# Performance work log

Hardware: AMD Instinct MI355X
Metric: run time of the kernel (lower is better)

The kernel has to match this reference:

```python
import jax, jax.numpy as jnp
import numpy as np

NF = 64        # feature channels (nf == inter_channels == in_channels)
BURST = 14     # burst_size from Args
H = 128
W = 128
SCALE = 0.02   # weight init scale keeps softmax logits in a sane range


def conv1x1(x, w, b):
    # x: [B,C,H,W], w: [O,C], b: [O]
    return jnp.einsum('bchw,oc->bohw', x, w) + b[None, :, None, None]


def setup_inputs() -> dict:
    key = jax.random.key(0)
    ks = jax.random.split(key, 32)
    inp = {'aligned_fea': jax.random.normal(ks[0], (BURST, NF, H, W), dtype=jnp.float32)}
    names = ['gc', 'thc', 'phc', 'Wc', 'gh', 'thh', 'phh', 'Wh', 'gw', 'thw', 'phw', 'Ww']
    for i, n in enumerate(names):
        inp[n + '_w'] = SCALE * jax.random.normal(ks[1 + 2 * i], (NF, NF), dtype=jnp.float32)
        inp[n + '_b'] = SCALE * jax.random.normal(ks[2 + 2 * i], (NF,), dtype=jnp.float32)
    inp['fus_w'] = SCALE * jax.random.normal(ks[26], (NF, BURST * NF * 3), dtype=jnp.float32)
    inp['fus_b'] = SCALE * jax.random.normal(ks[27], (NF,), dtype=jnp.float32)
    return inp


def _forward(aligned_fea,
             gc_w, gc_b, thc_w, thc_b, phc_w, phc_b, Wc_w, Wc_b,
             gh_w, gh_b, thh_w, thh_b, phh_w, phh_b, Wh_w, Wh_b,
             gw_w, gw_b, thw_w, thw_b, phw_w, phw_b, Ww_w, Ww_b,
             fus_w, fus_b):
    B, C, h, w = aligned_fea.shape  # [14, 64, 128, 128]
    x = aligned_fea
    ref = aligned_fea[0:1]  # [1,C,H,W]

    # ---- channel non-local (self) ----
    g = conv1x1(x, gc_w, gc_b).reshape(B, C, h * w)
    th = conv1x1(x, thc_w, thc_b).reshape(B, C, h * w)
    ph = conv1x1(x, phc_w, phc_b).reshape(B, C, h * w)
    f = jnp.einsum('bcn,bdn->bcd', th, ph)            # [B,C,C]
    f = jax.nn.softmax(f, axis=1)                     # softmax over dim=1 as in torch
    y = jnp.einsum('bcd,bdn->bcn', f, g)              # [B,C,HW]
    y = jnp.transpose(y, (0, 2, 1)).reshape(B, C, h, w)  # permute+view as in torch
    zc = conv1x1(y, Wc_w, Wc_b) + x

    # ---- height non-local (cross with ref) ----
    g = conv1x1(x, gh_w, gh_b).reshape(B, h, C * w)
    th = conv1x1(ref, thh_w, thh_b).reshape(1, h, C * w)
    ph = conv1x1(x, phh_w, phh_b).reshape(B, h, C * w)
    f = jnp.einsum('bik,bjk->bij', jnp.broadcast_to(th, (B, h, C * w)), ph)  # [B,H,H]
    f = jax.nn.softmax(f, axis=1)
    y = jnp.einsum('bij,bjk->bik', f, g)              # [B,H,C*W]
    y = jnp.transpose(y, (0, 2, 1)).reshape(B, C, h, w)  # requires H == W
    zh = conv1x1(y, Wh_w, Wh_b) + x

    # ---- width non-local (cross with ref) ----
    g = conv1x1(x, gw_w, gw_b).reshape(B, w, C * h)
    th = conv1x1(ref, thw_w, thw_b).reshape(1, w, C * h)
    ph = conv1x1(x, phw_w, phw_b).reshape(B, w, C * h)
    f = jnp.einsum('bik,bjk->bij', jnp.broadcast_to(th, (B, w, C * h)), ph)  # [B,W,W]
    f = jax.nn.softmax(f, axis=1)
    y = jnp.einsum('bij,bjk->bik', f, g)              # [B,W,C*H]
    y = jnp.transpose(y, (0, 2, 1)).reshape(B, C, h, w)
    zw = conv1x1(y, Ww_w, Ww_b) + x

    # ---- fusion: cat frames along channel in order [c, h, w] ----
    feat = jnp.concatenate([zc.reshape(1, B * C, h, w),
                            zh.reshape(1, B * C, h, w),
                            zw.reshape(1, B * C, h, w)], axis=1)  # [1, 3*B*C, H, W]
    out = conv1x1(feat, fus_w, fus_b)
    return jnp.where(out >= 0, out, 0.2 * out)  # LeakyReLU(0.2)


def reference(aligned_fea,
              gc_w, gc_b, thc_w, thc_b, phc_w, phc_b, Wc_w, Wc_b,
              gh_w, gh_b, thh_w, thh_b, phh_w, phh_b, Wh_w, Wh_b,
              gw_w, gw_b, thw_w, thw_b, phw_w, phw_b, Ww_w, Ww_b,
              fus_w, fus_b):
    return _forward(aligned_fea,
                    gc_w, gc_b, thc_w, thc_b, phc_w, phc_b, Wc_w, Wc_b,
                    gh_w, gh_b, thh_w, thh_b, phh_w, phh_b, Wh_w, Wh_b,
                    gw_w, gw_b, thw_w, thw_b, phw_w, phw_b, Ww_w, Ww_b,
                    fus_w, fus_b)
```

## Files before the change

kernel.cpp:

```cpp
#include <hip/hip_runtime.h>

#define NF 64
#define BURST 14
#define NPIX 16384
#define CN (NF * NPIX)
#define LP 72

typedef short bf16x8 __attribute__((ext_vector_type(8)));
typedef float f32x4 __attribute__((ext_vector_type(4)));
typedef unsigned short us4 __attribute__((ext_vector_type(4)));

__device__ inline unsigned short f2bf(float f) {
    unsigned int u = __float_as_uint(f);
    return (unsigned short)((u + 0x7fffu + ((u >> 16) & 1u)) >> 16);
}
__device__ inline float bf2f(unsigned short u) {
    return __uint_as_float(((unsigned int)u) << 16);
}

__global__ __launch_bounds__(256) void cast_x(const float* __restrict__ X,
                                              unsigned short* __restrict__ XB,
                                              unsigned short* __restrict__ XT,
                                              float* __restrict__ S)
{
    __shared__ unsigned short Xs[128][LP];
    const int tid = threadIdx.x;
    const int p0 = blockIdx.x * 128;
    const int b = blockIdx.y;
    const size_t boff = (size_t)b * CN;
#pragma unroll
    for (int i = 0; i < 8; ++i) {
        const int id = tid + 256 * i;
        const int c = id >> 5, p4 = (id & 31) * 4;
        float4 v = *(const float4*)&X[boff + (size_t)c * NPIX + p0 + p4];
        us4 r;
        r.x = f2bf(v.x); r.y = f2bf(v.y); r.z = f2bf(v.z); r.w = f2bf(v.w);
        *(us4*)&XB[boff + (size_t)c * NPIX + p0 + p4] = r;
        Xs[p4 + 0][c] = r.x; Xs[p4 + 1][c] = r.y;
        Xs[p4 + 2][c] = r.z; Xs[p4 + 3][c] = r.w;
    }
    __syncthreads();
#pragma unroll
    for (int i = 0; i < 4; ++i) {
        const int id = tid + 256 * i;
        const int row = id >> 3, c8 = (id & 7) * 8;
        *(bf16x8*)&XT[boff + (size_t)(p0 + row) * 64 + c8] = *(const bf16x8*)&Xs[row][c8];
    }
    if (tid < 64) {
        float sv = 0.f;
        for (int pp = 0; pp < 128; ++pp) sv += bf2f(Xs[pp][tid]);
        atomicAdd(&S[(b * 2 + (p0 >= 8192 ? 1 : 0)) * 64 + tid], sv);
    }
}

__global__ __launch_bounds__(256) void precompute(
    const float* __restrict__ fus_w, const float* __restrict__ fus_b,
    const float* __restrict__ Wc, const float* __restrict__ bWc,
    const float* __restrict__ Wh, const float* __restrict__ bWh,
    const float* __restrict__ Ww, const float* __restrict__ bWw,
    const float* __restrict__ gcw, const float* __restrict__ ghw,
    const float* __restrict__ gww,
    unsigned short* __restrict__ M16, unsigned short* __restrict__ Wc16,
    float* __restrict__ cb, unsigned short* __restrict__ gT16)
{
    const int blk = blockIdx.x, tid = threadIdx.x;
    if (blk < 42) {
        __shared__ float Fl[64][65];
        __shared__ float Wl[64][65];
        const int g = blk / 14, b = blk % 14;
        const float* Wg = (g == 0) ? Wc : (g == 1) ? Wh : Ww;
#pragma unroll
        for (int i = 0; i < 4; ++i) {
            const int id = tid + 256 * i;
            const int r = id >> 4, c4 = (id & 15) * 4;
            float4 v = *(const float4*)&fus_w[r * 2688 + g * 896 + b * 64 + c4];
            Fl[r][c4] = v.x; Fl[r][c4 + 1] = v.y; Fl[r][c4 + 2] = v.z; Fl[r][c4 + 3] = v.w;
            float4 u = *(const float4*)&Wg[r * 64 + c4];
            Wl[r][c4] = u.x; Wl[r][c4 + 1] = u.y; Wl[r][c4 + 2] = u.z; Wl[r][c4 + 3] = u.w;
        }
        __syncthreads();
        const int o = tid & 63, qq = tid >> 6;
        float s[16];
#pragma unroll
        for (int i = 0; i < 16; ++i) s[i] = 0.f;
        for (int c2 = 0; c2 < 64; ++c2) {
            const float fv = Fl[o][c2];
#pragma unroll
            for (int i = 0; i < 16; ++i) s[i] += fv * Wl[c2][qq * 16 + i];
        }
        unsigned short* Mout = M16 + (size_t)blk * 4096;
#pragma unroll
        for (int i = 0; i < 16; i += 4) {
            us4 r4; r4.x = f2bf(s[i]); r4.y = f2bf(s[i + 1]); r4.z = f2bf(s[i + 2]); r4.w = f2bf(s[i + 3]);
            *(us4*)&Mout[o * 64 + qq * 16 + i] = r4;
        }
    } else if (blk < 98) {
        const int e0 = (blk - 42) * 1024 + tid * 4;
        const int o = e0 / 896, bc = e0 - o * 896;
        float4 a = *(const float4*)&fus_w[o * 2688 + bc];
        float4 b2 = *(const float4*)&fus_w[o * 2688 + 896 + bc];
        float4 c3 = *(const float4*)&fus_w[o * 2688 + 1792 + bc];
        us4 r;
        r.x = f2bf(a.x + b2.x + c3.x); r.y = f2bf(a.y + b2.y + c3.y);
        r.z = f2bf(a.z + b2.z + c3.z); r.w = f2bf(a.w + b2.w + c3.w);
        *(us4*)&Wc16[e0] = r;
    } else if (blk < 106) {
        __shared__ float red[256];
        const int o = (blk - 98) * 8 + (tid >> 5);
        const int lane = tid & 31;
        float s = 0.f;
        for (int t = 0; t < 84; ++t) {
            const int ch = lane + 32 * t;
            const int g = ch / 896, c2 = ch & 63;
            const float bg = (g == 0) ? bWc[c2] : (g == 1) ? bWh[c2] : bWw[c2];
            s += fus_w[o * 2688 + ch] * bg;
        }
        red[tid] = s;
        __syncthreads();
        if (tid < 8) {
            const int oo = (blk - 98) * 8 + tid;
            float t = fus_b[oo];
            for (int i = 0; i < 32; ++i) t += red[tid * 32 + i];
            cb[oo] = t;
        }
    } else {
        const int g = blk - 106;
        const float* wg = (g == 0) ? gcw : (g == 1) ? ghw : gww;
        unsigned short* dst = gT16 + (size_t)g * 4096;
        for (int e = tid; e < 4096; e += 256) {
            const int cp = e >> 6, d = e & 63;
            dst[e] = f2bf(wg[d * 64 + cp]);
        }
    }
}

__global__ __launch_bounds__(256) void gram(
    const unsigned short* __restrict__ XB, float* __restrict__ G)
{
    const int tid = threadIdx.x;
    const int w = tid >> 6, l = tid & 63, lm = l & 15, q = l >> 4;
    const int b = blockIdx.y, z = blockIdx.z;
    const unsigned short* A;
    const unsigned short* B;
    int k0, ksteps;
    if (z == 0) {
        A = XB + (size_t)b * CN; B = A;
        k0 = blockIdx.x * 2048; ksteps = 64;
    } else {
        const int dl = (z - 1) >> 1, dp = (z - 1) & 1;
        A = XB + (size_t)dl * 8192;
        B = XB + (size_t)b * CN + (size_t)dp * 8192;
        k0 = blockIdx.x * 1024; ksteps = 32;
    }
    const int mo = (w & 1) * 32, no = (w >> 1) * 32;
    f32x4 acc[2][2] = {};
    for (int ks = 0; ks < ksteps; ++ks) {
        const int k = k0 + ks * 32 + q * 8;
        bf16x8 a[2], bb[2];
#pragma unroll
        for (int mi = 0; mi < 2; ++mi) a[mi] = *(const bf16x8*)&A[(size_t)(mo + mi * 16 + lm) * NPIX + k];
#pragma unroll
        for (int ni = 0; ni < 2; ++ni) bb[ni] = *(const bf16x8*)&B[(size_t)(no + ni * 16 + lm) * NPIX + k];
#pragma unroll
        for (int mi = 0; mi < 2; ++mi)
#pragma unroll
            for (int ni = 0; ni < 2; ++ni)
                acc[mi][ni] = __builtin_amdgcn_mfma_f32_16x16x32_bf16(a[mi], bb[ni], acc[mi][ni], 0, 0, 0);
    }
    float* Gp = G + (size_t)(b * 5 + z) * 4096;
#pragma unroll
    for (int mi = 0; mi < 2; ++mi)
#pragma unroll
        for (int r = 0; r < 4; ++r)
#pragma unroll
            for (int ni = 0; ni < 2; ++ni)
                atomicAdd(&Gp[(mo + mi * 16 + q * 4 + r) * 64 + no + ni * 16 + lm], acc[mi][ni][r]);
}

__global__ __launch_bounds__(256) void sandwich(
    const float* __restrict__ thc_w, const float* __restrict__ phc_w,
    const float* __restrict__ thc_b, const float* __restrict__ phc_b,
    const float* __restrict__ thh_w, const float* __restrict__ phh_w,
    const float* __restrict__ thh_b, const float* __restrict__ phh_b,
    const float* __restrict__ thw_w, const float* __restrict__ phw_w,
    const float* __restrict__ thw_b, const float* __restrict__ phw_b,
    const float* __restrict__ G, const float* __restrict__ S,
    float* __restrict__ f1, float* __restrict__ f2)
{
    __shared__ float Wt[64][65], Wp[64][65], Gl[64][65], Tl[64][65];
    __shared__ float sth[64], sph[64], uu[64], vv[64], btl[64], bpl[64];
    const int b = blockIdx.x, y = blockIdx.y, tid = threadIdx.x;
    const float *Wth_g, *Wph_g, *bth_g, *bph_g, *Gp;
    float* outp; int dl = 0, dp = 0; float Kn;
    if (y == 0) {
        Wth_g = thc_w; Wph_g = phc_w; bth_g = thc_b; bph_g = phc_b;
        Gp = G + (size_t)(b * 5) * 4096; Kn = 16384.f;
        outp = f1 + (size_t)b * 4096;
    } else {
        const int part = (y - 1) / 4, e = (y - 1) & 3;
        dl = e >> 1; dp = e & 1;
        if (part == 0) { Wth_g = thh_w; Wph_g = phh_w; bth_g = thh_b; bph_g = phh_b; }
        else           { Wth_g = thw_w; Wph_g = phw_w; bth_g = thw_b; bph_g = phw_b; }
        Gp = G + (size_t)(b * 5 + 1 + e) * 4096; Kn = 8192.f;
        outp = f2 + (size_t)(part * 14 + b) * 16384;
    }
#pragma unroll
    for (int i = 0; i < 4; ++i) {
        const int id = tid + 256 * i;
        const int r = id >> 4, c4 = (id & 15) * 4;
        float4 v = *(const float4*)&Wth_g[r * 64 + c4];
        Wt[r][c4] = v.x; Wt[r][c4 + 1] = v.y; Wt[r][c4 + 2] = v.z; Wt[r][c4 + 3] = v.w;
        float4 u = *(const float4*)&Wph_g[r * 64 + c4];
        Wp[r][c4] = u.x; Wp[r][c4 + 1] = u.y; Wp[r][c4 + 2] = u.z; Wp[r][c4 + 3] = u.w;
        float4 g = *(const float4*)&Gp[r * 64 + c4];
        Gl[r][c4] = g.x; Gl[r][c4 + 1] = g.y; Gl[r][c4 + 2] = g.z; Gl[r][c4 + 3] = g.w;
    }
    if (tid < 64) {
        if (y == 0) { const float sf = S[b * 128 + tid] + S[b * 128 + 64 + tid]; sth[tid] = sf; sph[tid] = sf; }
        else { sth[tid] = S[dl * 64 + tid]; sph[tid] = S[b * 128 + dp * 64 + tid]; }
        btl[tid] = bth_g[tid]; bpl[tid] = bph_g[tid];
    }
    __syncthreads();
    if (tid < 64) {
        float su = 0.f, sv = 0.f;
        for (int c = 0; c < 64; ++c) { su += Wt[tid][c] * sth[c]; sv += Wp[tid][c] * sph[c]; }
        uu[tid] = su; vv[tid] = sv;
    }
    const int t = tid & 63, qq = tid >> 6;
    float r16[16];
#pragma unroll
    for (int i = 0; i < 16; ++i) r16[i] = 0.f;
    for (int c = 0; c < 64; ++c) {
        const float fv = Wt[t][c];
#pragma unroll
        for (int i = 0; i < 16; ++i) r16[i] += fv * Gl[c][qq * 16 + i];
    }
#pragma unroll
    for (int i = 0; i < 16; ++i) Tl[t][qq * 16 + i] = r16[i];
    __syncthreads();
#pragma unroll
    for (int i = 0; i < 16; ++i) r16[i] = 0.f;
    for (int c = 0; c < 64; ++c) {
        const float tv = Tl[t][c];
#pragma unroll
        for (int i = 0; i < 16; ++i) r16[i] += tv * Wp[qq * 16 + i][c];
    }
    if (y == 0) {
#pragma unroll
        for (int i = 0; i < 16; ++i) {
            const int d = qq * 16 + i;
            outp[t * 64 + d] = r16[i] + uu[t] * bpl[d] + btl[t] * vv[d] + Kn * btl[t] * bpl[d];
        }
    } else {
#pragma unroll
        for (int i = 0; i < 16; ++i) {
            const int tp = qq * 16 + i;
            outp[(2 * t + dl) * 128 + 2 * tp + dp] =
                r16[i] + uu[t] * bpl[tp] + btl[t] * vv[tp] + Kn * btl[t] * bpl[tp];
        }
    }
}

__global__ __launch_bounds__(256) void softmax_all(
    const float* __restrict__ f1, const float* __restrict__ f2,
    const float* __restrict__ gcb, const float* __restrict__ ghb,
    const float* __restrict__ gwb,
    unsigned short* __restrict__ o1, unsigned short* __restrict__ o2d,
    float* __restrict__ B1, float* __restrict__ B2)
{
    __shared__ float red[256];
    __shared__ float mxA[128], invA[128];
    __shared__ float bgl[64];
    const int bx = blockIdx.x, tid = threadIdx.x;
    if (bx < 14) {
        const float* Fb = f1 + (size_t)bx * 4096;
        unsigned short* Ob = o1 + (size_t)bx * 4096;
        if (tid < 64) bgl[tid] = gcb[tid];
        const int d = tid & 63, qq = tid >> 6;
        float mx = -1e30f;
        for (int c = qq * 16; c < qq * 16 + 16; ++c) mx = fmaxf(mx, Fb[c * 64 + d]);
        red[tid] = mx;
        __syncthreads();
        if (tid < 64) mxA[tid] = fmaxf(fmaxf(red[tid], red[64 + tid]), fmaxf(red[128 + tid], red[192 + tid]));
        __syncthreads();
        const float m = mxA[d];
        float s = 0.f;
        for (int c = qq * 16; c < qq * 16 + 16; ++c) s += __expf(Fb[c * 64 + d] - m);
        red[tid] = s;
        __syncthreads();
        if (tid < 64) invA[tid] = 1.f / (red[tid] + red[64 + tid] + red[128 + tid] + red[192 + tid]);
        __syncthreads();
        const int e0 = tid * 16;
        const int d0 = e0 & 63;
        float bp = 0.f;
#pragma unroll
        for (int i = 0; i < 16; i += 4) {
            us4 r4;
            float v0 = __expf(Fb[e0 + i] - mxA[d0 + i]) * invA[d0 + i];
            float v1 = __expf(Fb[e0 + i + 1] - mxA[d0 + i + 1]) * invA[d0 + i + 1];
            float v2 = __expf(Fb[e0 + i + 2] - mxA[d0 + i + 2]) * invA[d0 + i + 2];
            float v3 = __expf(Fb[e0 + i + 3] - mxA[d0 + i + 3]) * invA[d0 + i + 3];
            bp += v0 * bgl[d0 + i] + v1 * bgl[d0 + i + 1] + v2 * bgl[d0 + i + 2] + v3 * bgl[d0 + i + 3];
            r4.x = f2bf(v0); r4.y = f2bf(v1); r4.z = f2bf(v2); r4.w = f2bf(v3);
            *(us4*)&Ob[e0 + i] = r4;
        }
        red[tid] = bp;
        __syncthreads();
        if (tid < 64)
            B1[bx * 64 + tid] = red[tid * 4] + red[tid * 4 + 1] + red[tid * 4 + 2] + red[tid * 4 + 3];
    } else {
        const int idx = bx - 14;
        const float* Fb = f2 + (size_t)idx * 16384;
        if (tid < 64) bgl[tid] = (idx < 14) ? ghb[tid] : gwb[tid];
        const int j = tid & 127, ih = tid >> 7;
        float mx = -1e30f;
        for (int i = ih * 64; i < ih * 64 + 64; ++i) mx = fmaxf(mx, Fb[i * 128 + j]);
        red[tid] = mx;
        __syncthreads();
        if (tid < 128) mxA[tid] = fmaxf(red[tid], red[128 + tid]);
        __syncthreads();
        const float m = mxA[j];
        float s = 0.f;
        for (int i = ih * 64; i < ih * 64 + 64; ++i) s += __expf(Fb[i * 128 + j] - m);
        red[tid] = s;
        __syncthreads();
        if (tid < 128) invA[tid] = 1.f / (red[tid] + red[128 + tid]);
        __syncthreads();
        const int e0 = tid * 64;
        const int irow = tid >> 1;
        const int j0 = e0 & 127;
        unsigned short vt[2][32];
        float bp = 0.f;
        for (int ii = 0; ii < 64; ++ii) {
            const int jj = j0 + ii;
            const float v = __expf(Fb[e0 + ii] - mxA[jj]) * invA[jj];
            bp += v * bgl[jj >> 1];
            vt[jj & 1][ii >> 1] = f2bf(v);
        }
        unsigned short* Od = o2d + (size_t)idx * 16384 + irow * 64 + (j0 >> 1);
#pragma unroll
        for (int dlt = 0; dlt < 2; ++dlt)
#pragma unroll
            for (int ss = 0; ss < 32; ss += 4)
                *(us4*)&Od[dlt * 8192 + ss] = *(us4*)&vt[dlt][ss];
        red[tid] = bp;
        __syncthreads();
        if (tid < 128) B2[idx * 128 + tid] = red[2 * tid] + red[2 * tid + 1];
    }
}

__global__ __launch_bounds__(256) void kmat(
    const unsigned short* __restrict__ f16_1, const unsigned short* __restrict__ f2d,
    const unsigned short* __restrict__ gT16,
    unsigned short* __restrict__ K1, unsigned short* __restrict__ K2)
{
    const int b = blockIdx.x, y = blockIdx.y, tid = threadIdx.x;
    const int w = tid >> 6, l = tid & 63, lm = l & 15, q = l >> 4;
    if (y == 0) {
        const unsigned short* A = f16_1 + (size_t)b * 4096;
        const unsigned short* Bm = gT16;
        const int mo = (w & 1) * 32, no = (w >> 1) * 32;
        f32x4 acc[2][2] = {};
#pragma unroll
        for (int ks = 0; ks < 2; ++ks) {
            const int k = ks * 32 + q * 8;
            bf16x8 a[2], bb[2];
#pragma unroll
            for (int mi = 0; mi < 2; ++mi) a[mi] = *(const bf16x8*)&A[(mo + mi * 16 + lm) * 64 + k];
#pragma unroll
            for (int ni = 0; ni < 2; ++ni) bb[ni] = *(const bf16x8*)&Bm[(no + ni * 16 + lm) * 64 + k];
#pragma unroll
            for (int mi = 0; mi < 2; ++mi)
#pragma unroll
                for (int ni = 0; ni < 2; ++ni)
                    acc[mi][ni] = __builtin_amdgcn_mfma_f32_16x16x32_bf16(a[mi], bb[ni], acc[mi][ni], 0, 0, 0);
        }
        unsigned short* Kp = K1 + (size_t)b * 4096;
#pragma unroll
        for (int mi = 0; mi < 2; ++mi)
#pragma unroll
            for (int r = 0; r < 4; ++r)
#pragma unroll
                for (int ni = 0; ni < 2; ++ni)
                    Kp[(mo + mi * 16 + q * 4 + r) * 64 + no + ni * 16 + lm] = f2bf(acc[mi][ni][r]);
    } else {
        const int part = y - 1;
        const unsigned short* Bm = gT16 + (size_t)(1 + part) * 4096;
        unsigned short* Kp = K2 + (size_t)(part * 14 + b) * 16384;
        for (int dlt = 0; dlt < 2; ++dlt) {
            const unsigned short* A = f2d + (size_t)(part * 14 + b) * 16384 + dlt * 8192;
            const int mo = (w & 1) * 64, no = (w >> 1) * 32;
            f32x4 acc[4][2] = {};
#pragma unroll
            for (int ks = 0; ks < 2; ++ks) {
                const int k = ks * 32 + q * 8;
                bf16x8 a[4], bb[2];
#pragma unroll
                for (int mi = 0; mi < 4; ++mi) a[mi] = *(const bf16x8*)&A[(mo + mi * 16 + lm) * 64 + k];
#pragma unroll
                for (int ni = 0; ni < 2; ++ni) bb[ni] = *(const bf16x8*)&Bm[(no + ni * 16 + lm) * 64 + k];
#pragma unroll
                for (int mi = 0; mi < 4; ++mi)
#pragma unroll
                    for (int ni = 0; ni < 2; ++ni)
                        acc[mi][ni] = __builtin_amdgcn_mfma_f32_16x16x32_bf16(a[mi], bb[ni], acc[mi][ni], 0, 0, 0);
            }
#pragma unroll
            for (int mi = 0; mi < 4; ++mi)
#pragma unroll
                for (int r = 0; r < 4; ++r)
#pragma unroll
                    for (int ni = 0; ni < 2; ++ni)
                        Kp[dlt * 8192 + (mo + mi * 16 + q * 4 + r) * 64 + no + ni * 16 + lm] = f2bf(acc[mi][ni][r]);
        }
    }
}

__global__ __launch_bounds__(256) void fold_res(
    const unsigned short* __restrict__ Wcomb, const unsigned short* __restrict__ XT,
    float* __restrict__ Out)
{
    const int tid = threadIdx.x;
    const int w = tid >> 6, l = tid & 63, lm = l & 15, q = l >> 4;
    const int p0 = blockIdx.x * 64 + (w >> 1) * 32;
    const int oh = (w & 1) * 32;
    f32x4 acc[2][2] = {};
    for (int b = 0; b < 14; ++b) {
#pragma unroll
        for (int ks = 0; ks < 2; ++ks) {
            const int c0 = ks * 32 + q * 8;
            bf16x8 a[2], bb[2];
#pragma unroll
            for (int mi = 0; mi < 2; ++mi)
                a[mi] = *(const bf16x8*)&Wcomb[(oh + mi * 16 + lm) * 896 + b * 64 + c0];
#pragma unroll
            for (int ni = 0; ni < 2; ++ni)
                bb[ni] = *(const bf16x8*)&XT[(size_t)b * CN + (size_t)(p0 + ni * 16 + lm) * 64 + c0];
#pragma unroll
            for (int mi = 0; mi < 2; ++mi)
#pragma unroll
                for (int ni = 0; ni < 2; ++ni)
                    acc[mi][ni] = __builtin_amdgcn_mfma_f32_16x16x32_bf16(a[mi], bb[ni], acc[mi][ni], 0, 0, 0);
        }
    }
#pragma unroll
    for (int mi = 0; mi < 2; ++mi)
#pragma unroll
        for (int r = 0; r < 4; ++r) {
            const int o = oh + mi * 16 + q * 4 + r;
#pragma unroll
            for (int ni = 0; ni < 2; ++ni)
                Out[(size_t)o * NPIX + p0 + ni * 16 + lm] = acc[mi][ni][r];
        }
}

__global__ __launch_bounds__(256) void pv1k(
    const unsigned short* __restrict__ XT, const unsigned short* __restrict__ K1,
    const float* __restrict__ B1, unsigned short* __restrict__ Y)
{
    const int tid = threadIdx.x;
    const int w = tid >> 6, l = tid & 63, lm = l & 15, q = l >> 4;
    const int b = blockIdx.z;
    const int p0 = blockIdx.x * 256 + w * 64;
    const unsigned short* Xb = XT + (size_t)b * CN;
    const unsigned short* Kb = K1 + (size_t)b * 4096;
    f32x4 acc[4][4] = {};
#pragma unroll
    for (int ks = 0; ks < 2; ++ks) {
        const int c0 = ks * 32 + q * 8;
        bf16x8 a[4], bb[4];
#pragma unroll
        for (int mi = 0; mi < 4; ++mi) a[mi] = *(const bf16x8*)&Xb[(size_t)(p0 + mi * 16 + lm) * 64 + c0];
#pragma unroll
        for (int ni = 0; ni < 4; ++ni) bb[ni] = *(const bf16x8*)&Kb[(ni * 16 + lm) * 64 + c0];
#pragma unroll
        for (int mi = 0; mi < 4; ++mi)
#pragma unroll
            for (int ni = 0; ni < 4; ++ni)
                acc[mi][ni] = __builtin_amdgcn_mfma_f32_16x16x32_bf16(a[mi], bb[ni], acc[mi][ni], 0, 0, 0);
    }
    unsigned short* Yb = Y + (size_t)b * CN;
#pragma unroll
    for (int mi = 0; mi < 4; ++mi)
#pragma unroll
        for (int r = 0; r < 4; ++r) {
            const int p = p0 + mi * 16 + q * 4 + r;
#pragma unroll
            for (int ni = 0; ni < 4; ++ni) {
                const int c = ni * 16 + lm;
                Yb[(size_t)p * 64 + c] = f2bf(acc[mi][ni][r] + B1[b * 64 + c]);
            }
        }
}

__global__ __launch_bounds__(256) void pv23k(
    const unsigned short* __restrict__ XT, const unsigned short* __restrict__ K2,
    const float* __restrict__ B2, unsigned short* __restrict__ Y2,
    unsigned short* __restrict__ Y3)
{
    const int tid = threadIdx.x;
    const int w = tid >> 6, l = tid & 63, lm = l & 15, q = l >> 4;
    const int part = blockIdx.z / 14, b = blockIdx.z % 14;
    const int k00 = blockIdx.x * 256 + w * 64;
    const int i0 = blockIdx.y * 64;
    const unsigned short* Xb = XT + (size_t)b * CN;
    const unsigned short* Kb = K2 + (size_t)(part * 14 + b) * 16384;
    const float* Bb = B2 + (part * 14 + b) * 128;
    f32x4 acc[4][4] = {};
#pragma unroll
    for (int dlt = 0; dlt < 2; ++dlt) {
#pragma unroll
        for (int ks = 0; ks < 2; ++ks) {
            const int c0 = ks * 32 + q * 8;
            bf16x8 a[4], bb[4];
#pragma unroll
            for (int mi = 0; mi < 4; ++mi)
                a[mi] = *(const bf16x8*)&Xb[(size_t)(dlt * 8192 + k00 + mi * 16 + lm) * 64 + c0];
#pragma unroll
            for (int ni = 0; ni < 4; ++ni)
                bb[ni] = *(const bf16x8*)&Kb[dlt * 8192 + (i0 + ni * 16 + lm) * 64 + c0];
#pragma unroll
            for (int mi = 0; mi < 4; ++mi)
#pragma unroll
                for (int ni = 0; ni < 4; ++ni)
                    acc[mi][ni] = __builtin_amdgcn_mfma_f32_16x16x32_bf16(a[mi], bb[ni], acc[mi][ni], 0, 0, 0);
        }
    }
    unsigned short* Yb = (part ? Y3 : Y2) + (size_t)b * CN;
#pragma unroll
    for (int mi = 0; mi < 4; ++mi)
#pragma unroll
        for (int r = 0; r < 4; ++r) {
            const int k = k00 + mi * 16 + q * 4 + r;
#pragma unroll
            for (int ni = 0; ni < 4; ++ni) {
                const int ii = i0 + ni * 16 + lm;
                Yb[(size_t)k * 128 + ii] = f2bf(acc[mi][ni][r] + Bb[ii]);
            }
        }
}

__global__ __launch_bounds__(256) void yfold(
    const unsigned short* __restrict__ M16,
    const unsigned short* __restrict__ Y1, const unsigned short* __restrict__ Y2,
    const unsigned short* __restrict__ Y3, float* __restrict__ Out)
{
    __shared__ unsigned short As[64][LP];
    __shared__ unsigned short Ss[128][LP];
    const int tid = threadIdx.x;
    const int z = blockIdx.z;
    const unsigned short* Ap = M16 + (size_t)z * 14 * 4096;
    const unsigned short* S = (z == 0) ? Y1 : (z == 1) ? Y2 : Y3;
    const int p0 = blockIdx.x * 128;
    const int t0 = blockIdx.y * 7;
    const int w = tid >> 6, l = tid & 63, lm = l & 15, q = l >> 4;
    const int mo = (w & 1) * 32;
    const int no = (w >> 1) * 64;
    f32x4 acc[2][4] = {};

    for (int t = t0; t < t0 + 7; ++t) {
        __syncthreads();
#pragma unroll
        for (int i = 0; i < 2; ++i) {
            const int ch = tid + 256 * i;
            const int row = ch >> 3, c8 = (ch & 7) * 8;
            *(bf16x8*)&As[row][c8] = *(const bf16x8*)&Ap[(size_t)t * 4096 + (size_t)row * 64 + c8];
        }
#pragma unroll
        for (int i = 0; i < 4; ++i) {
            const int id = tid + 256 * i;
            const int c = id & 63, p8 = (id >> 6) * 8;
            bf16x8 v = *(const bf16x8*)&S[(size_t)t * CN + (size_t)c * NPIX + p0 + p8];
#pragma unroll
            for (int j = 0; j < 8; ++j) Ss[p8 + j][c] = (unsigned short)v[j];
        }
        __syncthreads();
#pragma unroll
        for (int ks = 0; ks < 2; ++ks) {
            const int c0 = ks * 32 + q * 8;
            bf16x8 a[2], bb[4];
#pragma unroll
            for (int mi = 0; mi < 2; ++mi) a[mi] = *(const bf16x8*)&As[mo + mi * 16 + lm][c0];
#pragma unroll
            for (int ni = 0; ni < 4; ++ni) bb[ni] = *(const bf16x8*)&Ss[no + ni * 16 + lm][c0];
#pragma unroll
            for (int mi = 0; mi < 2; ++mi)
#pragma unroll
                for (int ni = 0; ni < 4; ++ni)
                    acc[mi][ni] = __builtin_amdgcn_mfma_f32_16x16x32_bf16(a[mi], bb[ni], acc[mi][ni], 0, 0, 0);
        }
    }
#pragma unroll
    for (int mi = 0; mi < 2; ++mi)
#pragma unroll
        for (int r = 0; r < 4; ++r) {
            const int o = mo + mi * 16 + q * 4 + r;
#pragma unroll
            for (int ni = 0; ni < 4; ++ni)
                atomicAdd(&Out[(size_t)o * NPIX + p0 + no + ni * 16 + lm], acc[mi][ni][r]);
        }
}

__global__ __launch_bounds__(256) void leaky_cb(float* __restrict__ O, const float* __restrict__ cb)
{
    const int i = blockIdx.x * 256 + threadIdx.x;
    float4 v = ((float4*)O)[i];
    const float b = cb[(i * 4) >> 14];
    v.x += b; v.y += b; v.z += b; v.w += b;
    v.x = v.x >= 0.f ? v.x : 0.2f * v.x;
    v.y = v.y >= 0.f ? v.y : 0.2f * v.y;
    v.z = v.z >= 0.f ? v.z : 0.2f * v.z;
    v.w = v.w >= 0.f ? v.w : 0.2f * v.w;
    ((float4*)O)[i] = v;
}

extern "C" void kernel_launch(void* const* d_in, const int* in_sizes, int n_in,
                              void* d_out, int out_size, void* d_ws, size_t ws_size,
                              hipStream_t stream)
{
    const float* x     = (const float*)d_in[0];
    const float* gc_w  = (const float*)d_in[1];
    const float* gc_b  = (const float*)d_in[2];
    const float* thc_w = (const float*)d_in[3];
    const float* thc_b = (const float*)d_in[4];
    const float* phc_w = (const float*)d_in[5];
    const float* phc_b = (const float*)d_in[6];
    const float* Wc_w  = (const float*)d_in[7];
    const float* Wc_b  = (const float*)d_in[8];
    const float* gh_w  = (const float*)d_in[9];
    const float* gh_b  = (const float*)d_in[10];
    const float* thh_w = (const float*)d_in[11];
    const float* thh_b = (const float*)d_in[12];
    const float* phh_w = (const float*)d_in[13];
    const float* phh_b = (const float*)d_in[14];
    const float* Wh_w  = (const float*)d_in[15];
    const float* Wh_b  = (const float*)d_in[16];
    const float* gw_w  = (const float*)d_in[17];
    const float* gw_b  = (const float*)d_in[18];
    const float* thw_w = (const float*)d_in[19];
    const float* thw_b = (const float*)d_in[20];
    const float* phw_w = (const float*)d_in[21];
    const float* phw_b = (const float*)d_in[22];
    const float* Ww_w  = (const float*)d_in[23];
    const float* Ww_b  = (const float*)d_in[24];
    const float* fus_w = (const float*)d_in[25];
    const float* fus_b = (const float*)d_in[26];

    float* out = (float*)d_out;

    char* p = (char*)d_ws;
    unsigned short* xb   = (unsigned short*)p; p += (size_t)BURST * CN * 2;
    unsigned short* xT   = (unsigned short*)p; p += (size_t)BURST * CN * 2;
    unsigned short* y1   = (unsigned short*)p; p += (size_t)BURST * CN * 2;
    unsigned short* y2   = (unsigned short*)p; p += (size_t)BURST * CN * 2;
    unsigned short* y3   = (unsigned short*)p; p += (size_t)BURST * CN * 2;
    float*          Gbuf = (float*)p;          p += (size_t)BURST * 5 * 4096 * 4;
    float*          sbuf = (float*)p;          p += (size_t)BURST * 2 * 64 * 4;
    float*          f1b  = (float*)p;          p += (size_t)BURST * 4096 * 4;
    float*          f2b  = (float*)p;          p += (size_t)2 * BURST * 16384 * 4;
    unsigned short* f16_1 = (unsigned short*)p; p += (size_t)BURST * 4096 * 2;
    unsigned short* f2d  = (unsigned short*)p; p += (size_t)2 * BURST * 16384 * 2;
    unsigned short* K1   = (unsigned short*)p; p += (size_t)BURST * 4096 * 2;
    unsigned short* K2   = (unsigned short*)p; p += (size_t)2 * BURST * 16384 * 2;
    float*          B1   = (float*)p;          p += (size_t)BURST * 64 * 4;
    float*          B2   = (float*)p;          p += (size_t)2 * BURST * 128 * 4;
    unsigned short* M16  = (unsigned short*)p; p += (size_t)42 * 4096 * 2;
    unsigned short* Wc16 = (unsigned short*)p; p += (size_t)64 * 896 * 2;
    unsigned short* gT16 = (unsigned short*)p; p += (size_t)3 * 4096 * 2;
    float*          cbv  = (float*)p;          p += 256;

    hipMemsetAsync(Gbuf, 0, ((size_t)BURST * 5 * 4096 + (size_t)BURST * 2 * 64) * 4, stream);

    cast_x<<<dim3(128, 14), 256, 0, stream>>>(x, xb, xT, sbuf);
    precompute<<<109, 256, 0, stream>>>(fus_w, fus_b, Wc_w, Wc_b, Wh_w, Wh_b, Ww_w, Ww_b,
                                        gc_w, gh_w, gw_w, M16, Wc16, cbv, gT16);
    gram<<<dim3(8, 14, 5), 256, 0, stream>>>(xb, Gbuf);
    sandwich<<<dim3(14, 9), 256, 0, stream>>>(
        thc_w, phc_w, thc_b, phc_b, thh_w, phh_w, thh_b, phh_b,
        thw_w, phw_w, thw_b, phw_b, Gbuf, sbuf, f1b, f2b);
    softmax_all<<<42, 256, 0, stream>>>(f1b, f2b, gc_b, gh_b, gw_b,
                                        f16_1, f2d, B1, B2);
    kmat<<<dim3(14, 3), 256, 0, stream>>>(f16_1, f2d, gT16, K1, K2);
    fold_res<<<256, 256, 0, stream>>>(Wc16, xT, out);
    pv1k<<<dim3(64, 1, BURST), 256, 0, stream>>>(xT, K1, B1, y1);
    pv23k<<<dim3(32, 2, 2 * BURST), 256, 0, stream>>>(xT, K2, B2, y2, y3);
    yfold<<<dim3(128, 2, 3), 256, 0, stream>>>(M16, y1, y2, y3, out);
    leaky_cb<<<1024, 256, 0, stream>>>(out, cbv);
}
```

Before: 360.1 us.

## Fuse gram variants into one pass with split-K partials and a reduce kernel

The gram kernel now computes all five Gram products per frame in one pass. Each block loads the frame rows and reference rows once and reuses them across five accumulator sets, where before it launched a separate z-slice per product. Float atomics are replaced by per-K-slice partial stores into a scratch buffer that aliases y1, followed by a separate reduction kernel. The channel-sum in cast_x is also spread across all 256 threads with a shared-memory reduction. The trade-offs are higher register pressure from five accumulator sets, an extra kernel launch, and extra scratch traffic.

After: 331.0 us. 1.09x faster.

```diff
diff --git a/kernel.cpp b/kernel.cpp
--- a/kernel.cpp
+++ b/kernel.cpp
@@ -24,6 +24,7 @@
                                               float* __restrict__ S)
 {
     __shared__ unsigned short Xs[128][LP];
+    __shared__ float red[256];
     const int tid = threadIdx.x;
     const int p0 = blockIdx.x * 128;
     const int b = blockIdx.y;
@@ -46,10 +47,16 @@
         const int row = id >> 3, c8 = (id & 7) * 8;
         *(bf16x8*)&XT[boff + (size_t)(p0 + row) * 64 + c8] = *(const bf16x8*)&Xs[row][c8];
     }
-    if (tid < 64) {
+    {
+        const int c = tid & 63, qq = tid >> 6;
         float sv = 0.f;
-        for (int pp = 0; pp < 128; ++pp) sv += bf2f(Xs[pp][tid]);
-        atomicAdd(&S[(b * 2 + (p0 >= 8192 ? 1 : 0)) * 64 + tid], sv);
+        for (int pp = qq * 32; pp < qq * 32 + 32; ++pp) sv += bf2f(Xs[pp][c]);
+        red[tid] = sv;
+        __syncthreads();
+        if (tid < 64) {
+            const float t = red[tid] + red[64 + tid] + red[128 + tid] + red[192 + tid];
+            atomicAdd(&S[(b * 2 + (p0 >= 8192 ? 1 : 0)) * 64 + tid], t);
+        }
     }
 }
 
@@ -135,46 +142,60 @@
 }
 
 __global__ __launch_bounds__(256) void gram(
-    const unsigned short* __restrict__ XB, float* __restrict__ G)
+    const unsigned short* __restrict__ XB, float* __restrict__ Gpart)
 {
     const int tid = threadIdx.x;
     const int w = tid >> 6, l = tid & 63, lm = l & 15, q = l >> 4;
-    const int b = blockIdx.y, z = blockIdx.z;
-    const unsigned short* A;
-    const unsigned short* B;
-    int k0, ksteps;
-    if (z == 0) {
-        A = XB + (size_t)b * CN; B = A;
-        k0 = blockIdx.x * 2048; ksteps = 64;
-    } else {
-        const int dl = (z - 1) >> 1, dp = (z - 1) & 1;
-        A = XB + (size_t)dl * 8192;
-        B = XB + (size_t)b * CN + (size_t)dp * 8192;
-        k0 = blockIdx.x * 1024; ksteps = 32;
-    }
+    const int b = blockIdx.y;
     const int mo = (w & 1) * 32, no = (w >> 1) * 32;
-    f32x4 acc[2][2] = {};
-    for (int ks = 0; ks < ksteps; ++ks) {
-        const int k = k0 + ks * 32 + q * 8;
-        bf16x8 a[2], bb[2];
-#pragma unroll
-        for (int mi = 0; mi < 2; ++mi) a[mi] = *(const bf16x8*)&A[(size_t)(mo + mi * 16 + lm) * NPIX + k];
-#pragma unroll
-        for (int ni = 0; ni < 2; ++ni) bb[ni] = *(const bf16x8*)&B[(size_t)(no + ni * 16 + lm) * NPIX + k];
+    const unsigned short* P = XB;
+    const unsigned short* Q = XB + (size_t)b * CN;
+    f32x4 a0[2][2] = {}, a1[2][2] = {}, a2[2][2] = {}, a3[2][2] = {}, a4[2][2] = {};
+#pragma unroll 2
+    for (int ki = 0; ki < 8; ++ki) {
+        const int k = blockIdx.x * 256 + ki * 32 + q * 8;
+        bf16x8 p0[2], p1[2], qm0[2], qm1[2], qn0[2], qn1[2];
+#pragma unroll
+        for (int mi = 0; mi < 2; ++mi) {
+            const size_t rm = (size_t)(mo + mi * 16 + lm) * NPIX;
+            const size_t rn = (size_t)(no + mi * 16 + lm) * NPIX;
+            p0[mi]  = *(const bf16x8*)&P[rm + k];
+            p1[mi]  = *(const bf16x8*)&P[rm + 8192 + k];
+            qm0[mi] = *(const bf16x8*)&Q[rm + k];
+            qm1[mi] = *(const bf16x8*)&Q[rm + 8192 + k];
+            qn0[mi] = *(const bf16x8*)&Q[rn + k];
+            qn1[mi] = *(const bf16x8*)&Q[rn + 8192 + k];
+        }
 #pragma unroll
         for (int mi = 0; mi < 2; ++mi)
 #pragma unroll
-            for (int ni = 0; ni < 2; ++ni)
-                acc[mi][ni] = __builtin_amdgcn_mfma_f32_16x16x32_bf16(a[mi], bb[ni], acc[mi][ni], 0, 0, 0);
-    }
-    float* Gp = G + (size_t)(b * 5 + z) * 4096;
-#pragma unroll
-    for (int mi = 0; mi < 2; ++mi)
-#pragma unroll
-        for (int r = 0; r < 4; ++r)
-#pragma unroll
-            for (int ni = 0; ni < 2; ++ni)
-                atomicAdd(&Gp[(mo + mi * 16 + q * 4 + r) * 64 + no + ni * 16 + lm], acc[mi][ni][r]);
+            for (int ni = 0; ni < 2; ++ni) {
+                a0[mi][ni] = __builtin_amdgcn_mfma_f32_16x16x32_bf16(qm0[mi], qn0[ni], a0[mi][ni], 0, 0, 0);
+                a0[mi][ni] = __builtin_amdgcn_mfma_f32_16x16x32_bf16(qm1[mi], qn1[ni], a0[mi][ni], 0, 0, 0);
+                a1[mi][ni] = __builtin_amdgcn_mfma_f32_16x16x32_bf16(p0[mi], qn0[ni], a1[mi][ni], 0, 0, 0);
+                a2[mi][ni] = __builtin_amdgcn_mfma_f32_16x16x32_bf16(p0[mi], qn1[ni], a2[mi][ni], 0, 0, 0);
+                a3[mi][ni] = __builtin_amdgcn_mfma_f32_16x16x32_bf16(p1[mi], qn0[ni], a3[mi][ni], 0, 0, 0);
+                a4[mi][ni] = __builtin_amdgcn_mfma_f32_16x16x32_bf16(p1[mi], qn1[ni], a4[mi][ni], 0, 0, 0);
+            }
+    }
+    float* Gp = Gpart + (size_t)(blockIdx.x * 14 + b) * 5 * 4096;
+#define STORE_Z(zidx, ACC)                                                     \
+    for (int mi = 0; mi < 2; ++mi)                                             \
+        for (int r = 0; r < 4; ++r)                                            \
+            for (int ni = 0; ni < 2; ++ni)                                     \
+                Gp[zidx * 4096 + (mo + mi * 16 + q * 4 + r) * 64 + no + ni * 16 + lm] = ACC[mi][ni][r];
+    STORE_Z(0, a0) STORE_Z(1, a1) STORE_Z(2, a2) STORE_Z(3, a3) STORE_Z(4, a4)
+#undef STORE_Z
+}
+
+__global__ __launch_bounds__(256) void gram_reduce(
+    const float* __restrict__ Gpart, float* __restrict__ G)
+{
+    const int e = blockIdx.x * 256 + threadIdx.x;
+    float s = 0.f;
+#pragma unroll
+    for (int ks = 0; ks < 32; ++ks) s += Gpart[(size_t)ks * 286720 + e];
+    G[e] = s;
 }
 
 __global__ __launch_bounds__(256) void sandwich(
@@ -669,12 +690,15 @@
     unsigned short* gT16 = (unsigned short*)p; p += (size_t)3 * 4096 * 2;
     float*          cbv  = (float*)p;          p += 256;
 
-    hipMemsetAsync(Gbuf, 0, ((size_t)BURST * 5 * 4096 + (size_t)BURST * 2 * 64) * 4, stream);
+    float* Gpart = (float*)y1;
+
+    hipMemsetAsync(sbuf, 0, (size_t)BURST * 2 * 64 * 4, stream);
 
     cast_x<<<dim3(128, 14), 256, 0, stream>>>(x, xb, xT, sbuf);
     precompute<<<109, 256, 0, stream>>>(fus_w, fus_b, Wc_w, Wc_b, Wh_w, Wh_b, Ww_w, Ww_b,
                                         gc_w, gh_w, gw_w, M16, Wc16, cbv, gT16);
-    gram<<<dim3(8, 14, 5), 256, 0, stream>>>(xb, Gbuf);
+    gram<<<dim3(32, 14), 256, 0, stream>>>(xb, Gpart);
+    gram_reduce<<<1120, 256, 0, stream>>>(Gpart, Gbuf);
     sandwich<<<dim3(14, 9), 256, 0, stream>>>(
         thc_w, phc_w, thc_b, phc_b, thh_w, phh_w, thh_b, phh_b,
         thw_w, phw_w, thw_b, phw_b, Gbuf, sbuf, f1b, f2b);
```
